# Optimization experiments

Hardware: AMD Instinct MI355X
Metric: run time of the kernel (lower is better)

Reference implementation:

```python
import jax, jax.numpy as jnp
import numpy as np

EPS = 1e-8
K = 3  # num_neighbors

def setup_inputs() -> dict:
    key = jax.random.key(0)
    k1, k2, k3, k4 = jax.random.split(key, 4)
    n, B, m, C = 16384, 8, 2048, 128
    return {
        "unknown": jax.random.normal(k1, (n, 3), dtype=jnp.float32),
        "known": jax.random.normal(k2, (B, m, 3), dtype=jnp.float32),
        "batch_inds": jax.random.randint(k3, (n,), 0, B),
        "known_feats": jax.random.normal(k4, (B, C, m), dtype=jnp.float32),
    }

def reference(unknown, known, batch_inds, known_feats):
    # unknown: (n,3); known: (B,m,3); batch_inds: (n,); known_feats: (B,C,m)
    kg = known[batch_inds]                                   # (n,m,3) gather per-query scene
    d2 = jnp.sum((unknown[:, None, :] - kg) ** 2, axis=-1)   # (n,m) squared L2
    neg_d2, idx = jax.lax.top_k(-d2, K)                      # 3 nearest (sorted ascending dist)
    dist = jnp.sqrt(jnp.maximum(-neg_d2, 0.0))               # (n,K)
    dist_recip = 1.0 / (dist + EPS)
    weight = dist_recip / jnp.sum(dist_recip, axis=-1, keepdims=True)  # (n,K)
    # gather neighbor features: (n,K,C)
    feats = known_feats[batch_inds[:, None], :, idx]
    out = jnp.einsum('nkc,nk->nc', feats, weight)            # (n,C)
    return out[:, :, None]                                   # (n,C,1)
```

## Files before the change

kernel.cpp:

```cpp
#include <hip/hip_runtime.h>

#define NPTS 16384
#define NB   8
#define NM   2048
#define NC   128
#define EPSF 1e-8f

#define TQ   16
#define QPB  16
#define GX   160

#define MERGE3(d, j) do {                                       \
    const bool _b0 = (d) < D0;                                  \
    const bool _b1 = (d) < D1;                                  \
    const bool _b2 = (d) < D2;                                  \
    const float _n0 = fminf((d), D0);                           \
    const float _n1 = __builtin_amdgcn_fmed3f(D0, D1, (d));     \
    const float _n2 = __builtin_amdgcn_fmed3f(D1, D2, (d));     \
    I2 = _b1 ? I1 : (_b2 ? (j) : I2);                           \
    I1 = _b0 ? I0 : (_b1 ? (j) : I1);                           \
    I0 = _b0 ? (j) : I0;                                        \
    D0 = _n0; D1 = _n1; D2 = _n2;                               \
} while (0)

#define MERGE_DI(ed, ei) do {                                           \
    const bool _b2 = ((ed) < D2) || (((ed) == D2) && ((ei) < I2));      \
    const bool _b1 = ((ed) < D1) || (((ed) == D1) && ((ei) < I1));      \
    const bool _b0 = ((ed) < D0) || (((ed) == D0) && ((ei) < I0));      \
    D2 = _b1 ? D1 : (_b2 ? (ed) : D2);                                  \
    I2 = _b1 ? I1 : (_b2 ? (ei) : I2);                                  \
    D1 = _b0 ? D0 : (_b1 ? (ed) : D1);                                  \
    I1 = _b0 ? I0 : (_b1 ? (ei) : I1);                                  \
    D0 = _b0 ? (ed) : D0;                                               \
    I0 = _b0 ? (ei) : I0;                                               \
} while (0)

__global__ __launch_bounds__(256) void transpose_feats(const float* __restrict__ feats,
                                                       float* __restrict__ ws) {
    __shared__ float tile[64][NC + 1];
    const int b   = blockIdx.y;
    const int j0  = blockIdx.x * 64;
    const int tid = threadIdx.x;
    const float* src = feats + (size_t)b * NC * NM;
    float*       dst = ws    + (size_t)b * NM * NC;
    {
        const int j  = tid & 63;
        const int c4 = tid >> 6;
#pragma unroll
        for (int c0 = 0; c0 < NC; c0 += 4) {
            const int c = c0 + c4;
            tile[j][c] = src[(size_t)c * NM + j0 + j];
        }
    }
    __syncthreads();
    {
        const int c  = tid & 127;
        const int j2 = tid >> 7;
#pragma unroll
        for (int jj = 0; jj < 64; jj += 2) {
            const int j = jj + j2;
            dst[(size_t)(j0 + j) * NC + c] = tile[j][c];
        }
    }
}

__global__ __launch_bounds__(256, 4) void fused(const float* __restrict__ unknown,
                                                const float* __restrict__ known,
                                                const int*   __restrict__ binds,
                                                const float* __restrict__ feats,
                                                const float* __restrict__ ws,
                                                const int useT,
                                                float* __restrict__ out) {
    __shared__ float2 kx2[NM / 2];
    __shared__ float2 ky2[NM / 2];
    __shared__ float2 kz2[NM / 2];
    __shared__ int qlist[QPB];
    __shared__ int wsum[4];

    const int tid  = threadIdx.x;
    const int b    = blockIdx.y;
    const int x    = blockIdx.x;
    const int lane = tid & 63;
    const int wave = tid >> 6;

    const int4* b4 = (const int4*)binds;
    int myCnt = 0;
#pragma unroll
    for (int r = 0; r < 16; ++r) {
        const int4 v = b4[tid * 16 + r];
        myCnt += (v.x == b) + (v.y == b) + (v.z == b) + (v.w == b);
    }
    int inc = myCnt;
#pragma unroll
    for (int off = 1; off <= 32; off <<= 1) {
        const int n = __shfl_up(inc, off);
        if (lane >= off) inc += n;
    }
    if (lane == 63) wsum[wave] = inc;
    __syncthreads();
    int wbase = 0;
    for (int w = 0; w < wave; ++w) wbase += wsum[w];
    const int exPre = wbase + inc - myCnt;
    const int segN  = wsum[0] + wsum[1] + wsum[2] + wsum[3];

    if (x * QPB >= segN) return;

    {
        const float* kb = known + (size_t)b * NM * 3;
        for (int p = tid; p < NM / 2; p += 256) {
            const float* s = kb + p * 6;
            float2 vx, vy, vz;
            vx.x = s[0]; vy.x = s[1]; vz.x = s[2];
            vx.y = s[3]; vy.y = s[4]; vz.y = s[5];
            kx2[p] = vx; ky2[p] = vy; kz2[p] = vz;
        }
    }

    const int qi = tid >> 4;
    const int t  = tid & 15;

    for (int w0 = x * QPB; w0 < segN; w0 += GX * QPB) {
        __syncthreads();
        if (exPre < w0 + QPB && exPre + myCnt > w0) {
            int rank = exPre;
#pragma unroll
            for (int r = 0; r < 16; ++r) {
                const int4 v = b4[tid * 16 + r];
                const int base = tid * 64 + r * 4;
                if (v.x == b) { if (rank >= w0 && rank < w0 + QPB) qlist[rank - w0] = base + 0; ++rank; }
                if (v.y == b) { if (rank >= w0 && rank < w0 + QPB) qlist[rank - w0] = base + 1; ++rank; }
                if (v.z == b) { if (rank >= w0 && rank < w0 + QPB) qlist[rank - w0] = base + 2; ++rank; }
                if (v.w == b) { if (rank >= w0 && rank < w0 + QPB) qlist[rank - w0] = base + 3; ++rank; }
            }
        }
        __syncthreads();

        const int valid = (segN - w0 < QPB) ? (segN - w0) : QPB;
        const int kq    = (qi < valid) ? qi : 0;
        const int p     = qlist[kq];
        const float ux = unknown[p * 3 + 0];
        const float uy = unknown[p * 3 + 1];
        const float uz = unknown[p * 3 + 2];

        float D0 = __builtin_inff(), D1 = __builtin_inff(), D2 = __builtin_inff();
        int   I0 = NM, I1 = NM, I2 = NM;

#pragma unroll 8
        for (int i = 0; i < NM / (2 * TQ); ++i) {
            const int pr = (i << 4) | t;
            const float2 vx = kx2[pr];
            const float2 vy = ky2[pr];
            const float2 vz = kz2[pr];
            const int jLo = pr << 1;
            const float dx0 = __fsub_rn(ux, vx.x);
            const float dy0 = __fsub_rn(uy, vy.x);
            const float dz0 = __fsub_rn(uz, vz.x);
            const float dx1 = __fsub_rn(ux, vx.y);
            const float dy1 = __fsub_rn(uy, vy.y);
            const float dz1 = __fsub_rn(uz, vz.y);
            const float dLo = __fadd_rn(__fadd_rn(__fmul_rn(dx0, dx0), __fmul_rn(dy0, dy0)),
                                        __fmul_rn(dz0, dz0));
            const float dHi = __fadd_rn(__fadd_rn(__fmul_rn(dx1, dx1), __fmul_rn(dy1, dy1)),
                                        __fmul_rn(dz1, dz1));
            MERGE3(dLo, jLo);
            MERGE3(dHi, jLo + 1);
        }

#pragma unroll
        for (int off = 8; off >= 1; off >>= 1) {
            const float e0d = __shfl_down(D0, off);
            const float e1d = __shfl_down(D1, off);
            const float e2d = __shfl_down(D2, off);
            const int   e0i = __shfl_down(I0, off);
            const int   e1i = __shfl_down(I1, off);
            const int   e2i = __shfl_down(I2, off);
            MERGE_DI(e0d, e0i);
            MERGE_DI(e1d, e1i);
            MERGE_DI(e2d, e2i);
        }
        const int src = lane & ~15;
        D0 = __shfl(D0, src); D1 = __shfl(D1, src); D2 = __shfl(D2, src);
        I0 = __shfl(I0, src); I1 = __shfl(I1, src); I2 = __shfl(I2, src);

        const float t0 = 1.0f / (sqrtf(D0) + EPSF);
        const float t1 = 1.0f / (sqrtf(D1) + EPSF);
        const float t2 = 1.0f / (sqrtf(D2) + EPSF);
        const float s  = t0 + t1 + t2;
        const float w0w = t0 / s, w1w = t1 / s, w2w = t2 / s;

        if (useT) {
            const float* fb2 = ws + (size_t)b * NM * NC;
            const float4* r0 = (const float4*)(fb2 + (size_t)I0 * NC);
            const float4* r1 = (const float4*)(fb2 + (size_t)I1 * NC);
            const float4* r2 = (const float4*)(fb2 + (size_t)I2 * NC);
            float4* op = (float4*)(out + (size_t)p * NC);
#pragma unroll
            for (int k = 0; k < 2; ++k) {
                const int c4 = t + (k << 4);
                const float4 f0 = r0[c4];
                const float4 f1 = r1[c4];
                const float4 f2 = r2[c4];
                float4 o;
                o.x = w0w * f0.x + w1w * f1.x + w2w * f2.x;
                o.y = w0w * f0.y + w1w * f1.y + w2w * f2.y;
                o.z = w0w * f0.z + w1w * f1.z + w2w * f2.z;
                o.w = w0w * f0.w + w1w * f1.w + w2w * f2.w;
                op[c4] = o;
            }
        } else {
            const float* fb = feats + (size_t)b * NC * NM;
#pragma unroll
            for (int k = 0; k < 8; ++k) {
                const int c = t + (k << 4);
                const float* fc = fb + (size_t)c * NM;
                const float f0 = fc[I0];
                const float f1 = fc[I1];
                const float f2 = fc[I2];
                out[(size_t)p * NC + c] = w0w * f0 + w1w * f1 + w2w * f2;
            }
        }
    }
}

extern "C" void kernel_launch(void* const* d_in, const int* in_sizes, int n_in,
                              void* d_out, int out_size, void* d_ws, size_t ws_size,
                              hipStream_t stream) {
    const float* unknown = (const float*)d_in[0];
    const float* known   = (const float*)d_in[1];
    const int*   binds   = (const int*)d_in[2];
    const float* feats   = (const float*)d_in[3];
    float*       out     = (float*)d_out;

    const size_t tsz = (size_t)NB * NC * NM * sizeof(float);
    const int useT = (d_ws != nullptr && ws_size >= tsz) ? 1 : 0;
    float* ws = (float*)d_ws;

    if (useT) {
        transpose_feats<<<dim3(NM / 64, NB), 256, 0, stream>>>(feats, ws);
    }
    fused<<<dim3(GX, NB), 256, 0, stream>>>(unknown, known, binds, feats, ws, useT, out);
}
```

Before: 110.8 us.

## Precompute per-batch query lists in prep kernel and use float4 LDS layout

Merges the feature transpose with a new compaction pass that builds per-batch query index lists in workspace, so the main kernel no longer rescans batch_inds in every block. The main fast kernel reads the precomputed list and count, exits idle blocks early, and stores known points as float4 SoA in shared memory to cut LDS load instructions. The cost is an extra workspace region and a fixed QSTRIDE capacity of 2560 queries per batch, which could overflow for skewed batch distributions.

```diff
diff --git a/kernel.cpp b/kernel.cpp
--- a/kernel.cpp
+++ b/kernel.cpp
@@ -9,6 +9,7 @@
 #define TQ   16
 #define QPB  16
 #define GX   160
+#define QSTRIDE 2560
 
 #define MERGE3(d, j) do {                                       \
     const bool _b0 = (d) < D0;                                  \
@@ -35,31 +36,184 @@
     I0 = _b0 ? (ei) : I0;                                               \
 } while (0)
 
-__global__ __launch_bounds__(256) void transpose_feats(const float* __restrict__ feats,
-                                                       float* __restrict__ ws) {
+__global__ __launch_bounds__(256) void prep(const float* __restrict__ feats,
+                                            const int*   __restrict__ binds,
+                                            float* __restrict__ ws) {
     __shared__ float tile[64][NC + 1];
+    __shared__ int wsum[4];
     const int b   = blockIdx.y;
-    const int j0  = blockIdx.x * 64;
     const int tid = threadIdx.x;
-    const float* src = feats + (size_t)b * NC * NM;
-    float*       dst = ws    + (size_t)b * NM * NC;
+
+    if (blockIdx.x < NM / 64) {
+        const int j0  = blockIdx.x * 64;
+        const float* src = feats + (size_t)b * NC * NM;
+        float*       dst = ws    + (size_t)b * NM * NC;
+        {
+            const int j  = tid & 63;
+            const int c4 = tid >> 6;
+#pragma unroll
+            for (int c0 = 0; c0 < NC; c0 += 4) {
+                const int c = c0 + c4;
+                tile[j][c] = src[(size_t)c * NM + j0 + j];
+            }
+        }
+        __syncthreads();
+        {
+            const int c  = tid & 127;
+            const int j2 = tid >> 7;
+#pragma unroll
+            for (int jj = 0; jj < 64; jj += 2) {
+                const int j = jj + j2;
+                dst[(size_t)(j0 + j) * NC + c] = tile[j][c];
+            }
+        }
+    } else {
+        int* qws = (int*)(ws + (size_t)NB * NM * NC);
+        const int lane = tid & 63;
+        const int wave = tid >> 6;
+        const int4* b4 = (const int4*)binds;
+        int myCnt = 0;
+#pragma unroll
+        for (int r = 0; r < 16; ++r) {
+            const int4 v = b4[tid * 16 + r];
+            myCnt += (v.x == b) + (v.y == b) + (v.z == b) + (v.w == b);
+        }
+        int inc = myCnt;
+#pragma unroll
+        for (int off = 1; off <= 32; off <<= 1) {
+            const int n = __shfl_up(inc, off);
+            if (lane >= off) inc += n;
+        }
+        if (lane == 63) wsum[wave] = inc;
+        __syncthreads();
+        int wbase = 0;
+        for (int w = 0; w < wave; ++w) wbase += wsum[w];
+        int rank = wbase + inc - myCnt;
+        int* qb = qws + b * QSTRIDE;
+#pragma unroll
+        for (int r = 0; r < 16; ++r) {
+            const int4 v = b4[tid * 16 + r];
+            const int base = tid * 64 + r * 4;
+            if (v.x == b) qb[rank++] = base + 0;
+            if (v.y == b) qb[rank++] = base + 1;
+            if (v.z == b) qb[rank++] = base + 2;
+            if (v.w == b) qb[rank++] = base + 3;
+        }
+        if (tid == 255) qws[NB * QSTRIDE + b] = wbase + inc;
+    }
+}
+
+__global__ __launch_bounds__(256, 4) void fused_fast(const float* __restrict__ unknown,
+                                                     const float* __restrict__ known,
+                                                     const float* __restrict__ ws,
+                                                     float* __restrict__ out) {
+    __shared__ float4 kx4[NM / 4];
+    __shared__ float4 ky4[NM / 4];
+    __shared__ float4 kz4[NM / 4];
+
+    const int tid = threadIdx.x;
+    const int b   = blockIdx.y;
+    const int x   = blockIdx.x;
+
+    const int* qws = (const int*)(ws + (size_t)NB * NM * NC);
+    const int segN = qws[NB * QSTRIDE + b];
+    if (x * QPB >= segN) return;
+
     {
-        const int j  = tid & 63;
-        const int c4 = tid >> 6;
-#pragma unroll
-        for (int c0 = 0; c0 < NC; c0 += 4) {
-            const int c = c0 + c4;
-            tile[j][c] = src[(size_t)c * NM + j0 + j];
+        const float* kb = known + (size_t)b * NM * 3;
+        for (int q = tid; q < NM / 4; q += 256) {
+            const float* s = kb + q * 12;
+            kx4[q] = make_float4(s[0], s[3], s[6], s[9]);
+            ky4[q] = make_float4(s[1], s[4], s[7], s[10]);
+            kz4[q] = make_float4(s[2], s[5], s[8], s[11]);
         }
     }
     __syncthreads();
-    {
-        const int c  = tid & 127;
-        const int j2 = tid >> 7;
-#pragma unroll
-        for (int jj = 0; jj < 64; jj += 2) {
-            const int j = jj + j2;
-            dst[(size_t)(j0 + j) * NC + c] = tile[j][c];
+
+    const int qi = tid >> 4;
+    const int t  = tid & 15;
+    const int* qb = qws + b * QSTRIDE;
+
+    for (int w0 = x * QPB; w0 < segN; w0 += GX * QPB) {
+        const int valid = (segN - w0 < QPB) ? (segN - w0) : QPB;
+        const int kq    = (qi < valid) ? qi : 0;
+        const int p     = qb[w0 + kq];
+        const float ux = unknown[p * 3 + 0];
+        const float uy = unknown[p * 3 + 1];
+        const float uz = unknown[p * 3 + 2];
+
+        float D0 = __builtin_inff(), D1 = __builtin_inff(), D2 = __builtin_inff();
+        int   I0 = NM, I1 = NM, I2 = NM;
+
+#pragma unroll 4
+        for (int i = 0; i < NM / (4 * TQ); ++i) {
+            const int q = (i << 4) | t;
+            const float4 vx = kx4[q];
+            const float4 vy = ky4[q];
+            const float4 vz = kz4[q];
+            const int j = q << 2;
+            {
+                const float dx = __fsub_rn(ux, vx.x), dy = __fsub_rn(uy, vy.x), dz = __fsub_rn(uz, vz.x);
+                const float d  = __fadd_rn(__fadd_rn(__fmul_rn(dx, dx), __fmul_rn(dy, dy)), __fmul_rn(dz, dz));
+                MERGE3(d, j);
+            }
+            {
+                const float dx = __fsub_rn(ux, vx.y), dy = __fsub_rn(uy, vy.y), dz = __fsub_rn(uz, vz.y);
+                const float d  = __fadd_rn(__fadd_rn(__fmul_rn(dx, dx), __fmul_rn(dy, dy)), __fmul_rn(dz, dz));
+                MERGE3(d, j + 1);
+            }
+            {
+                const float dx = __fsub_rn(ux, vx.z), dy = __fsub_rn(uy, vy.z), dz = __fsub_rn(uz, vz.z);
+                const float d  = __fadd_rn(__fadd_rn(__fmul_rn(dx, dx), __fmul_rn(dy, dy)), __fmul_rn(dz, dz));
+                MERGE3(d, j + 2);
+            }
+            {
+                const float dx = __fsub_rn(ux, vx.w), dy = __fsub_rn(uy, vy.w), dz = __fsub_rn(uz, vz.w);
+                const float d  = __fadd_rn(__fadd_rn(__fmul_rn(dx, dx), __fmul_rn(dy, dy)), __fmul_rn(dz, dz));
+                MERGE3(d, j + 3);
+            }
+        }
+
+        const int lane = tid & 63;
+#pragma unroll
+        for (int off = 8; off >= 1; off >>= 1) {
+            const float e0d = __shfl_down(D0, off);
+            const float e1d = __shfl_down(D1, off);
+            const float e2d = __shfl_down(D2, off);
+            const int   e0i = __shfl_down(I0, off);
+            const int   e1i = __shfl_down(I1, off);
+            const int   e2i = __shfl_down(I2, off);
+            MERGE_DI(e0d, e0i);
+            MERGE_DI(e1d, e1i);
+            MERGE_DI(e2d, e2i);
+        }
+        const int src = lane & ~15;
+        D0 = __shfl(D0, src); D1 = __shfl(D1, src); D2 = __shfl(D2, src);
+        I0 = __shfl(I0, src); I1 = __shfl(I1, src); I2 = __shfl(I2, src);
+
+        const float t0 = 1.0f / (sqrtf(D0) + EPSF);
+        const float t1 = 1.0f / (sqrtf(D1) + EPSF);
+        const float t2 = 1.0f / (sqrtf(D2) + EPSF);
+        const float s  = t0 + t1 + t2;
+        const float w0w = t0 / s, w1w = t1 / s, w2w = t2 / s;
+
+        const float* fb2 = ws + (size_t)b * NM * NC;
+        const float4* r0 = (const float4*)(fb2 + (size_t)I0 * NC);
+        const float4* r1 = (const float4*)(fb2 + (size_t)I1 * NC);
+        const float4* r2 = (const float4*)(fb2 + (size_t)I2 * NC);
+        float4* op = (float4*)(out + (size_t)p * NC);
+#pragma unroll
+        for (int k = 0; k < 2; ++k) {
+            const int c4 = t + (k << 4);
+            const float4 f0 = r0[c4];
+            const float4 f1 = r1[c4];
+            const float4 f2 = r2[c4];
+            float4 o;
+            o.x = w0w * f0.x + w1w * f1.x + w2w * f2.x;
+            o.y = w0w * f0.y + w1w * f1.y + w2w * f2.y;
+            o.z = w0w * f0.z + w1w * f1.z + w2w * f2.z;
+            o.w = w0w * f0.w + w1w * f1.w + w2w * f2.w;
+            op[c4] = o;
         }
     }
 }
@@ -68,8 +222,6 @@
                                                 const float* __restrict__ known,
                                                 const int*   __restrict__ binds,
                                                 const float* __restrict__ feats,
-                                                const float* __restrict__ ws,
-                                                const int useT,
                                                 float* __restrict__ out) {
     __shared__ float2 kx2[NM / 2];
     __shared__ float2 ky2[NM / 2];
@@ -188,36 +340,15 @@
         const float s  = t0 + t1 + t2;
         const float w0w = t0 / s, w1w = t1 / s, w2w = t2 / s;
 
-        if (useT) {
-            const float* fb2 = ws + (size_t)b * NM * NC;
-            const float4* r0 = (const float4*)(fb2 + (size_t)I0 * NC);
-            const float4* r1 = (const float4*)(fb2 + (size_t)I1 * NC);
-            const float4* r2 = (const float4*)(fb2 + (size_t)I2 * NC);
-            float4* op = (float4*)(out + (size_t)p * NC);
-#pragma unroll
-            for (int k = 0; k < 2; ++k) {
-                const int c4 = t + (k << 4);
-                const float4 f0 = r0[c4];
-                const float4 f1 = r1[c4];
-                const float4 f2 = r2[c4];
-                float4 o;
-                o.x = w0w * f0.x + w1w * f1.x + w2w * f2.x;
-                o.y = w0w * f0.y + w1w * f1.y + w2w * f2.y;
-                o.z = w0w * f0.z + w1w * f1.z + w2w * f2.z;
-                o.w = w0w * f0.w + w1w * f1.w + w2w * f2.w;
-                op[c4] = o;
-            }
-        } else {
-            const float* fb = feats + (size_t)b * NC * NM;
-#pragma unroll
-            for (int k = 0; k < 8; ++k) {
-                const int c = t + (k << 4);
-                const float* fc = fb + (size_t)c * NM;
-                const float f0 = fc[I0];
-                const float f1 = fc[I1];
-                const float f2 = fc[I2];
-                out[(size_t)p * NC + c] = w0w * f0 + w1w * f1 + w2w * f2;
-            }
+        const float* fb = feats + (size_t)b * NC * NM;
+#pragma unroll
+        for (int k = 0; k < 8; ++k) {
+            const int c = t + (k << 4);
+            const float* fc = fb + (size_t)c * NM;
+            const float f0 = fc[I0];
+            const float f1 = fc[I1];
+            const float f2 = fc[I2];
+            out[(size_t)p * NC + c] = w0w * f0 + w1w * f1 + w2w * f2;
         }
     }
 }
@@ -231,12 +362,14 @@
     const float* feats   = (const float*)d_in[3];
     float*       out     = (float*)d_out;
 
-    const size_t tsz = (size_t)NB * NC * NM * sizeof(float);
-    const int useT = (d_ws != nullptr && ws_size >= tsz) ? 1 : 0;
+    const size_t fsz = (size_t)NB * NC * NM * sizeof(float);
+    const size_t qsz = (size_t)(NB * QSTRIDE + NB) * sizeof(int);
     float* ws = (float*)d_ws;
 
-    if (useT) {
-        transpose_feats<<<dim3(NM / 64, NB), 256, 0, stream>>>(feats, ws);
-    }
-    fused<<<dim3(GX, NB), 256, 0, stream>>>(unknown, known, binds, feats, ws, useT, out);
+    if (ws != nullptr && ws_size >= fsz + qsz) {
+        prep<<<dim3(NM / 64 + 1, NB), 256, 0, stream>>>(feats, binds, ws);
+        fused_fast<<<dim3(GX, NB), 256, 0, stream>>>(unknown, known, ws, out);
+    } else {
+        fused<<<dim3(GX, NB), 256, 0, stream>>>(unknown, known, binds, feats, out);
+    }
 }
```

New measurement: 102.0 us. 1.09x faster.
